# Kernel optimization log

Measured on AMD Instinct MI355X. Metric: run time of the kernel, lower is better.

The kernel has to match this reference:

```python
import math
import jax, jax.numpy as jnp
import numpy as np

EMB = 512
HEADS = 8
NEG_INF = -1e30  # stand-in for -inf that stays finite under softmax


def setup_inputs() -> dict:
    key = jax.random.key(0)
    ks = jax.random.split(key, 6)
    b, t, e, h = 2, 2048, EMB, HEADS
    s = 1.0 / math.sqrt(e)
    return {
        "x": jax.random.normal(ks[0], (b, t, e), dtype=jnp.float32),
        "Wk": jax.random.normal(ks[1], (h * e, e), dtype=jnp.float32) * s,
        "Wq": jax.random.normal(ks[2], (h * e, e), dtype=jnp.float32) * s,
        "Wv": jax.random.normal(ks[3], (h * e, e), dtype=jnp.float32) * s,
        "Wc": jax.random.normal(ks[4], (e, h * e), dtype=jnp.float32) * s,
        "bc": jax.random.normal(ks[5], (e,), dtype=jnp.float32) * 0.01,
    }


def reference(x, Wk, Wq, Wv, Wc, bc):
    b, t, e = x.shape
    h = HEADS
    # projections: Linear(e, h*e) -> (b, t, h, e) -> (b, h, t, e)
    k = (x @ Wk.T).reshape(b, t, h, e).transpose(0, 2, 1, 3)
    q = (x @ Wq.T).reshape(b, t, h, e).transpose(0, 2, 1, 3)
    v = (x @ Wv.T).reshape(b, t, h, e).transpose(0, 2, 1, 3)
    scores = jnp.einsum("bhqe,bhke->bhqk", q, k) / math.sqrt(e)
    # causal mask: strict upper triangle (offset=1) set to -inf
    causal = jnp.tril(jnp.ones((t, t), dtype=bool))  # True where allowed
    scores = jnp.where(causal, scores, NEG_INF)
    weights = jax.nn.softmax(scores, axis=-1)
    out = jnp.einsum("bhqk,bhke->bhqe", weights, v)  # (b, h, t, e)
    out = out.transpose(0, 2, 1, 3).reshape(b, t, h * e)
    return out @ Wc.T + bc
```

## Files before the change

### kernel.cpp

```cpp
#include <hip/hip_runtime.h>

typedef unsigned short u16;
typedef __attribute__((ext_vector_type(4))) short short4v;
typedef __attribute__((ext_vector_type(8))) short short8;
typedef __attribute__((ext_vector_type(4))) float floatx4;

#define GLL16(g, l) __builtin_amdgcn_global_load_lds( \
    (const __attribute__((address_space(1))) void*)(g), \
    (__attribute__((address_space(3))) void*)(l), 16, 0, 0)

__device__ __forceinline__ float b2f(u16 h) {
    union { unsigned u; float f; } v; v.u = ((unsigned)h) << 16; return v.f;
}
__device__ __forceinline__ u16 f2b(float f) {
    union { float f; unsigned u; } v; v.f = f;
    unsigned r = v.u + 0x7fffu + ((v.u >> 16) & 1u);
    return (u16)(r >> 16);
}
__device__ __forceinline__ float launder(float f) {
    return fminf(fmaxf(f, -30000.0f), 30000.0f);
}
__device__ __forceinline__ short8 cvt8(floatx4 a, floatx4 b) {
    short8 v;
    v[0] = (short)f2b(a[0]); v[1] = (short)f2b(a[1]);
    v[2] = (short)f2b(a[2]); v[3] = (short)f2b(a[3]);
    v[4] = (short)f2b(b[0]); v[5] = (short)f2b(b[1]);
    v[6] = (short)f2b(b[2]); v[7] = (short)f2b(b[3]);
    return v;
}

__device__ __forceinline__ int sniff_block(const u16* __restrict__ xs)
{
    __shared__ int cnt;
    if (threadIdx.x == 0) cnt = 0;
    __syncthreads();
    int local = 0;
    for (int i = threadIdx.x; i < 4096; i += 256) {
        const int ex = (xs[i] >> 7) & 0xFF;
        if (ex >= 0x90) ++local;
    }
    if (local) atomicAdd(&cnt, local);
    __syncthreads();
    return cnt > 256;
}

__device__ __forceinline__ void conv_one(const void* __restrict__ raw,
                                         u16* __restrict__ dst, int n, int isf32)
{
    int i = (blockIdx.x * 256 + threadIdx.x) * 8;
    const int stride = gridDim.x * 256 * 8;
    if (isf32) {
        const float* s = (const float*)raw;
        for (; i < n; i += stride)
            *(short8*)(dst + i) = cvt8(*(const floatx4*)(s + i),
                                       *(const floatx4*)(s + i + 4));
    } else {
        const u16* s = (const u16*)raw;
        for (; i < n; i += stride)
            *(short8*)(dst + i) = *(const short8*)(s + i);
    }
}

__global__ __launch_bounds__(256)
void convert4(const void* r0, const void* r1, const void* r2, const void* r3,
              u16* d0, u16* d1, u16* d2, u16* d3, int n, const u16* xs)
{
    const int isf32 = sniff_block(xs);
    const int z = blockIdx.y;
    const void* raw = (z == 0) ? r0 : (z == 1) ? r1 : (z == 2) ? r2 : r3;
    u16* dst        = (z == 0) ? d0 : (z == 1) ? d1 : (z == 2) ? d2 : d3;
    conv_one(raw, dst, n, isf32);
}

__global__ __launch_bounds__(256)
void convert2(const void* r0, const void* r1, u16* d0, u16* d1,
              int n0, int n1, const u16* xs, int* flagp)
{
    const int isf32 = sniff_block(xs);
    if (blockIdx.x == 0 && blockIdx.y == 0 && threadIdx.x == 0) flagp[0] = isf32;
    if (blockIdx.y == 0) conv_one(r0, d0, n0, isf32);
    else                 conv_one(r1, d1, n1, isf32);
}

__global__ __launch_bounds__(256, 2)
void gemm_qkv(const u16* __restrict__ A,
              const u16* __restrict__ B0, const u16* __restrict__ B1, const u16* __restrict__ B2,
              u16* __restrict__ C0, u16* __restrict__ C1, u16* __restrict__ VTout)
{
    const int bid = (blockIdx.x & 7) * 384 + (blockIdx.x >> 3);
    const int z  = bid % 3;
    const int t  = bid / 3;
    const int mx = t & 31;
    const int my = t >> 5;

    const u16* B = (z == 0) ? B0 : ((z == 1) ? B1 : B2);

    __shared__ u16 smem[128 * 136];

    const int tid  = threadIdx.x;
    const int wave = tid >> 6;
    const int lane = tid & 63;
    const int c16  = lane & 15;
    const int quad = lane >> 4;
    const int m0 = mx * 128;
    const int n0 = my * 128;
    const int wm = (wave >> 1) * 64;
    const int wn = (wave & 1) * 64;

    floatx4 acc[4][4] = {};

    const int srow = wave * 32 + (lane >> 2);
    const int scol = (lane & 3) * 8;
    const u16* Ag = A + (size_t)(m0 + srow) * 512 + scol;
    const u16* Bg = B + (size_t)(n0 + srow) * 512 + scol;
    const int woff = (wave * 32) * 32;

    GLL16(Ag,            smem + woff);
    GLL16(Ag + 16 * 512, smem + woff + 16 * 32);
    GLL16(Bg,            smem + 8192 + woff);
    GLL16(Bg + 16 * 512, smem + 8192 + woff + 16 * 32);
    int cur = 0;

    for (int k0 = 0; k0 < 512; k0 += 32) {
        __syncthreads();
        u16* Asc = smem + cur * 4096;
        u16* Bsc = smem + 8192 + cur * 4096;

        if (k0 + 32 < 512) {
            u16* Asn = smem + (cur ^ 1) * 4096;
            u16* Bsn = smem + 8192 + (cur ^ 1) * 4096;
            GLL16(Ag + k0 + 32,            Asn + woff);
            GLL16(Ag + k0 + 32 + 16 * 512, Asn + woff + 16 * 32);
            GLL16(Bg + k0 + 32,            Bsn + woff);
            GLL16(Bg + k0 + 32 + 16 * 512, Bsn + woff + 16 * 32);
        }

        short8 af[4], bf[4];
#pragma unroll
        for (int i = 0; i < 4; ++i)
            af[i] = *(const short8*)&Asc[(wm + i * 16 + c16) * 32 + quad * 8];
#pragma unroll
        for (int i = 0; i < 4; ++i)
            bf[i] = *(const short8*)&Bsc[(wn + i * 16 + c16) * 32 + quad * 8];
#pragma unroll
        for (int i = 0; i < 4; ++i)
#pragma unroll
            for (int j = 0; j < 4; ++j)
                acc[i][j] = __builtin_amdgcn_mfma_f32_16x16x32_bf16(af[i], bf[j], acc[i][j], 0, 0, 0);
        cur ^= 1;
    }

    __syncthreads();

    if (z == 2) {
#pragma unroll
        for (int i = 0; i < 4; ++i)
#pragma unroll
            for (int j = 0; j < 4; ++j) {
                const int lc = wn + j * 16 + c16;
#pragma unroll
                for (int r = 0; r < 4; ++r) {
                    const int lr = wm + i * 16 + quad * 4 + r;
                    smem[lc * 136 + lr] = f2b(launder(acc[i][j][r]));
                }
            }
        __syncthreads();
        const int bq  = m0 >> 11;
        const int tt0 = m0 & 2047;
#pragma unroll
        for (int p = 0; p < 8; ++p) {
            const int lc  = p * 16 + (tid >> 4);
            const int seg = tid & 15;
            const short8 v = *(const short8*)&smem[lc * 136 + seg * 8];
            const int col = n0 + lc;
            const int hh = col >> 9, d = col & 511;
            *(short8*)&VTout[((size_t)((bq * 8 + hh) * 512 + d)) * 2048 + tt0 + seg * 8] = v;
        }
    } else {
        u16* C = (z == 0) ? C0 : C1;
#pragma unroll
        for (int i = 0; i < 4; ++i)
#pragma unroll
            for (int j = 0; j < 4; ++j) {
                const int lc = wn + j * 16 + c16;
#pragma unroll
                for (int r = 0; r < 4; ++r) {
                    const int lr = wm + i * 16 + quad * 4 + r;
                    smem[lr * 136 + lc] = f2b(launder(acc[i][j][r]));
                }
            }
        __syncthreads();
#pragma unroll
        for (int p = 0; p < 8; ++p) {
            const int lr  = p * 16 + (tid >> 4);
            const int seg = tid & 15;
            const short8 v = *(const short8*)&smem[lr * 136 + seg * 8];
            *(short8*)&C[(size_t)(m0 + lr) * 4096 + n0 + seg * 8] = v;
        }
    }
}

__global__ __launch_bounds__(256, 2)
void gemm_out(const u16* __restrict__ A, const u16* __restrict__ B,
              const u16* __restrict__ bias, const int* __restrict__ flagp,
              void* __restrict__ out)
{
    const int bid = (blockIdx.x & 7) * 64 + (blockIdx.x >> 3);
    const int nb = bid & 7;
    const int mb = bid >> 3;

    __shared__ u16 As[2][64 * 32];
    __shared__ u16 Bs[2][64 * 32];

    const int tid  = threadIdx.x;
    const int wave = tid >> 6;
    const int lane = tid & 63;
    const int c16  = lane & 15;
    const int quad = lane >> 4;
    const int m0 = mb * 64;
    const int n0 = nb * 64;
    const int wm = (wave >> 1) * 32;
    const int wn = (wave & 1) * 32;

    floatx4 acc[2][2] = {};

    const int srow = wave * 16 + (lane >> 2);
    const int scol = (lane & 3) * 8;
    const u16* Ag = A + (size_t)(m0 + srow) * 4096 + scol;
    const u16* Bg = B + (size_t)(n0 + srow) * 4096 + scol;
    const int woff = (wave * 16) * 32;

    GLL16(Ag, &As[0][woff]);
    GLL16(Bg, &Bs[0][woff]);
    int cur = 0;

    for (int k0 = 0; k0 < 4096; k0 += 32) {
        __syncthreads();

        if (k0 + 32 < 4096) {
            GLL16(Ag + k0 + 32, &As[cur ^ 1][woff]);
            GLL16(Bg + k0 + 32, &Bs[cur ^ 1][woff]);
        }

        short8 af[2], bf[2];
#pragma unroll
        for (int i = 0; i < 2; ++i)
            af[i] = *(const short8*)&As[cur][(wm + i * 16 + c16) * 32 + quad * 8];
#pragma unroll
        for (int j = 0; j < 2; ++j)
            bf[j] = *(const short8*)&Bs[cur][(wn + j * 16 + c16) * 32 + quad * 8];
#pragma unroll
        for (int i = 0; i < 2; ++i)
#pragma unroll
            for (int j = 0; j < 2; ++j)
                acc[i][j] = __builtin_amdgcn_mfma_f32_16x16x32_bf16(af[i], bf[j], acc[i][j], 0, 0, 0);
        cur ^= 1;
    }

    const int isf32 = flagp[0];
#pragma unroll
    for (int i = 0; i < 2; ++i)
#pragma unroll
        for (int j = 0; j < 2; ++j) {
            const int col = n0 + wn + j * 16 + c16;
            const float bv = b2f(bias[col]);
#pragma unroll
            for (int r = 0; r < 4; ++r) {
                const int row = m0 + wm + i * 16 + quad * 4 + r;
                const float val = launder(acc[i][j][r] + bv);
                if (isf32) ((float*)out)[(size_t)row * 512 + col] = val;
                else       ((u16*)out)[(size_t)row * 512 + col] = f2b(val);
            }
        }
}

#define LOG2E 1.4426950408889634f
#define SM_SCALE 0.044194173824159216f
#define PM 24.0f

__global__ __launch_bounds__(512, 2)
void flash_attn(const u16* __restrict__ Q, const u16* __restrict__ K,
                const u16* __restrict__ VT, u16* __restrict__ O)
{
    __shared__ u16 Ks[2][64 * 516];
    __shared__ u16 Ps[4][16 * 68];
    __shared__ float Lp[2][4][16];

    const int tid  = threadIdx.x;
    const int wave = tid >> 6;
    const int lane = tid & 63;
    const int c16  = lane & 15;
    const int quad = lane >> 4;
    const int g   = wave & 3;
    const int st2 = wave >> 2;

    const int x  = blockIdx.x;
    const int bh = x & 15;
    const int pr = x >> 4;
    const int b  = bh >> 3, h = bh & 7;

    const u16* Qh  = Q  + (size_t)b * 2048 * 4096 + (size_t)h * 512;
    const u16* Kh  = K  + (size_t)b * 2048 * 4096 + (size_t)h * 512;
    const u16* VTh = VT + (size_t)bh * 512 * 2048;
    u16*       Oh  = O  + (size_t)b * 2048 * 4096 + (size_t)h * 512;

#pragma unroll
    for (int i = 0; i < 8; ++i) {
        const int kr = wave * 8 + i;
        GLL16(Kh + (size_t)kr * 4096 + lane * 8, &Ks[0][kr * 516]);
    }
    int cur = 0;

    for (int pm = 0; pm < 2; ++pm) {
        const int qt = pm ? pr : (31 - pr);
        const int q0 = qt * 64;
        const int ntile = qt + 1;
        const int qrow = q0 + g * 16 + c16;
        const int rowq = q0 + g * 16 + quad * 4;

        short8 qf[16];
#pragma unroll
        for (int s = 0; s < 16; ++s)
            qf[s] = *(const short8*)(Qh + (size_t)qrow * 4096 + s * 32 + quad * 8);

        float l_i[4] = {0.0f, 0.0f, 0.0f, 0.0f};
        floatx4 oacc[4][4] = {};

        for (int t = 0; t < ntile; ++t) {
            const int kv0 = t * 64;
            __syncthreads();

            short8 vf[4][2];
            const u16* Vw = VTh + (size_t)(wave * 64) * 2048 + kv0;
#pragma unroll
            for (int dt = 0; dt < 4; ++dt)
#pragma unroll
                for (int ks = 0; ks < 2; ++ks)
                    vf[dt][ks] = *(const short8*)(Vw + (size_t)(dt * 16 + c16) * 2048 + ks * 32 + quad * 8);

            if (t + 1 < ntile || pm == 0) {
                const int knext = (t + 1 < ntile) ? (kv0 + 64) : 0;
#pragma unroll
                for (int i = 0; i < 8; ++i) {
                    const int kr = wave * 8 + i;
                    GLL16(Kh + (size_t)(knext + kr) * 4096 + lane * 8,
                          &Ks[cur ^ 1][kr * 516]);
                }
            }

            floatx4 sv0 = {}, sv1 = {};
            __builtin_amdgcn_s_setprio(1);
#pragma unroll
            for (int s = 0; s < 16; ++s) {
                short8 kf0 = *(const short8*)&Ks[cur][(st2 * 32 + c16) * 516 + s * 32 + quad * 8];
                short8 kf1 = *(const short8*)&Ks[cur][(st2 * 32 + 16 + c16) * 516 + s * 32 + quad * 8];
                sv0 = __builtin_amdgcn_mfma_f32_16x16x32_bf16(qf[s], kf0, sv0, 0, 0, 0);
                sv1 = __builtin_amdgcn_mfma_f32_16x16x32_bf16(qf[s], kf1, sv1, 0, 0, 0);
            }
            __builtin_amdgcn_s_setprio(0);

            const int col0 = kv0 + st2 * 32 + c16;
            if (t + 1 < ntile) {
#pragma unroll
                for (int r = 0; r < 4; ++r) {
                    const float p0 = exp2f((sv0[r] * SM_SCALE - PM) * LOG2E);
                    const float p1 = exp2f((sv1[r] * SM_SCALE - PM) * LOG2E);
                    l_i[r] += p0 + p1;
                    Ps[g][(quad * 4 + r) * 68 + st2 * 32 + c16]      = f2b(p0);
                    Ps[g][(quad * 4 + r) * 68 + st2 * 32 + 16 + c16] = f2b(p1);
                }
            } else {
#pragma unroll
                for (int r = 0; r < 4; ++r) {
                    const float p0 = (col0 > rowq + r)
                        ? 0.0f : exp2f((sv0[r] * SM_SCALE - PM) * LOG2E);
                    const float p1 = (col0 + 16 > rowq + r)
                        ? 0.0f : exp2f((sv1[r] * SM_SCALE - PM) * LOG2E);
                    l_i[r] += p0 + p1;
                    Ps[g][(quad * 4 + r) * 68 + st2 * 32 + c16]      = f2b(p0);
                    Ps[g][(quad * 4 + r) * 68 + st2 * 32 + 16 + c16] = f2b(p1);
                }
            }

            asm volatile("s_waitcnt lgkmcnt(0)" ::: "memory");
            __builtin_amdgcn_s_barrier();
            __builtin_amdgcn_sched_barrier(0);

            __builtin_amdgcn_s_setprio(1);
#pragma unroll
            for (int qg = 0; qg < 4; ++qg) {
                short8 pf0 = *(const short8*)&Ps[qg][c16 * 68 + quad * 8];
                short8 pf1 = *(const short8*)&Ps[qg][c16 * 68 + 32 + quad * 8];
#pragma unroll
                for (int dt = 0; dt < 4; ++dt) {
                    oacc[qg][dt] = __builtin_amdgcn_mfma_f32_16x16x32_bf16(pf0, vf[dt][0], oacc[qg][dt], 0, 0, 0);
                    oacc[qg][dt] = __builtin_amdgcn_mfma_f32_16x16x32_bf16(pf1, vf[dt][1], oacc[qg][dt], 0, 0, 0);
                }
            }
            __builtin_amdgcn_s_setprio(0);

            cur ^= 1;
        }

#pragma unroll
        for (int off = 1; off < 16; off <<= 1)
#pragma unroll
            for (int r = 0; r < 4; ++r)
                l_i[r] += __shfl_xor(l_i[r], off, 16);
        if (c16 == 0) {
#pragma unroll
            for (int r = 0; r < 4; ++r) Lp[st2][g][quad * 4 + r] = l_i[r];
        }
        __syncthreads();

#pragma unroll
        for (int qg = 0; qg < 4; ++qg) {
            float linv[4];
#pragma unroll
            for (int r = 0; r < 4; ++r)
                linv[r] = 1.0f / (Lp[0][qg][quad * 4 + r] + Lp[1][qg][quad * 4 + r]);
#pragma unroll
            for (int dt = 0; dt < 4; ++dt)
#pragma unroll
                for (int r = 0; r < 4; ++r)
                    Oh[(size_t)(q0 + qg * 16 + quad * 4 + r) * 4096 + wave * 64 + dt * 16 + c16] =
                        f2b(launder(oacc[qg][dt][r] * linv[r]));
        }
    }
}

extern "C" void kernel_launch(void* const* d_in, const int* in_sizes, int n_in,
                              void* d_out, int out_size, void* d_ws, size_t ws_size,
                              hipStream_t stream)
{
    const size_t SZ  = (size_t)4096 * 4096;
    const size_t SZh = (size_t)4096 * 512;

    u16* Qb  = (u16*)d_ws;
    u16* Kb  = Qb + SZ;
    u16* Vb  = Kb + SZ;
    u16* VTb = Vb + SZ;
    u16* Ob  = Vb;

    u16* xb  = Vb;
    u16* Wqb = Vb + SZh;
    u16* Wkb = Vb + 2 * SZh;
    u16* Wvb = Vb + 3 * SZh;

    u16* Wcb = Qb;
    u16* bcb = Qb + SZh;
    int* flagp = (int*)(Qb + 2 * SZh);

    const u16* xs = (const u16*)d_in[0];

    convert4<<<dim3(256, 4), 256, 0, stream>>>(
        d_in[0], d_in[2], d_in[1], d_in[3], xb, Wqb, Wkb, Wvb, (int)SZh, xs);

    gemm_qkv<<<dim3(3072), 256, 0, stream>>>(
        xb, Wqb, Wkb, Wvb, Qb, Kb, VTb);

    flash_attn<<<dim3(256), 512, 0, stream>>>(Qb, Kb, VTb, Ob);

    convert2<<<dim3(256, 2), 256, 0, stream>>>(
        d_in[4], d_in[5], Wcb, bcb, (int)SZh, 512, xs, flagp);

    gemm_out<<<dim3(512), 256, 0, stream>>>(Ob, Wcb, bcb, flagp, d_out);
}
```

Before: 370.9 us.

## Split output projection GEMM along K with a separate reduction kernel

The output projection GEMM (4096x512 output, K=4096) is split into four K-slices, each computed by blocks that now use 128x64 tiles. The blocks write fp32 partial sums into the K buffer, which is no longer needed at that point, and a new reduce kernel adds the four slices, applies the bias and converts the output. This is meant to fix the low block count and long serial K loop of the old 512-block kernel, at the cost of extra fp32 partial traffic and one more launch. The occupancy hint on both GEMM kernels is also raised from 2 to 4 blocks.

```diff
diff --git a/kernel.cpp b/kernel.cpp
--- a/kernel.cpp
+++ b/kernel.cpp
@@ -82,7 +82,7 @@
     else                 conv_one(r1, d1, n1, isf32);
 }
 
-__global__ __launch_bounds__(256, 2)
+__global__ __launch_bounds__(256, 4)
 void gemm_qkv(const u16* __restrict__ A,
               const u16* __restrict__ B0, const u16* __restrict__ B1, const u16* __restrict__ B2,
               u16* __restrict__ C0, u16* __restrict__ C1, u16* __restrict__ VTout)
@@ -200,16 +200,16 @@
     }
 }
 
-__global__ __launch_bounds__(256, 2)
-void gemm_out(const u16* __restrict__ A, const u16* __restrict__ B,
-              const u16* __restrict__ bias, const int* __restrict__ flagp,
-              void* __restrict__ out)
-{
-    const int bid = (blockIdx.x & 7) * 64 + (blockIdx.x >> 3);
+__global__ __launch_bounds__(256, 4)
+void gemm_out_partial(const u16* __restrict__ A, const u16* __restrict__ B,
+                      float* __restrict__ Pw)
+{
+    const int bid = blockIdx.x;
     const int nb = bid & 7;
-    const int mb = bid >> 3;
-
-    __shared__ u16 As[2][64 * 32];
+    const int ks = (bid >> 3) & 3;
+    const int mb = bid >> 5;
+
+    __shared__ u16 As[2][128 * 32];
     __shared__ u16 Bs[2][64 * 32];
 
     const int tid  = threadIdx.x;
@@ -217,61 +217,92 @@
     const int lane = tid & 63;
     const int c16  = lane & 15;
     const int quad = lane >> 4;
-    const int m0 = mb * 64;
+    const int m0 = mb * 128;
     const int n0 = nb * 64;
-    const int wm = (wave >> 1) * 32;
+    const int wm = (wave >> 1) * 64;
     const int wn = (wave & 1) * 32;
-
-    floatx4 acc[2][2] = {};
-
-    const int srow = wave * 16 + (lane >> 2);
-    const int scol = (lane & 3) * 8;
-    const u16* Ag = A + (size_t)(m0 + srow) * 4096 + scol;
-    const u16* Bg = B + (size_t)(n0 + srow) * 4096 + scol;
-    const int woff = (wave * 16) * 32;
-
-    GLL16(Ag, &As[0][woff]);
-    GLL16(Bg, &Bs[0][woff]);
+    const int kbase = ks * 1024;
+
+    floatx4 acc[4][2] = {};
+
+    const int srowA = wave * 32 + (lane >> 2);
+    const int srowB = wave * 16 + (lane >> 2);
+    const int scol  = (lane & 3) * 8;
+    const u16* Ag = A + (size_t)(m0 + srowA) * 4096 + kbase + scol;
+    const u16* Bg = B + (size_t)(n0 + srowB) * 4096 + kbase + scol;
+    const int woffA = (wave * 32) * 32;
+    const int woffB = (wave * 16) * 32;
+
+    GLL16(Ag,                     &As[0][woffA]);
+    GLL16(Ag + (size_t)16 * 4096, &As[0][woffA + 16 * 32]);
+    GLL16(Bg,                     &Bs[0][woffB]);
     int cur = 0;
 
-    for (int k0 = 0; k0 < 4096; k0 += 32) {
+    for (int k0 = 0; k0 < 1024; k0 += 32) {
         __syncthreads();
 
-        if (k0 + 32 < 4096) {
-            GLL16(Ag + k0 + 32, &As[cur ^ 1][woff]);
-            GLL16(Bg + k0 + 32, &Bs[cur ^ 1][woff]);
-        }
-
-        short8 af[2], bf[2];
-#pragma unroll
-        for (int i = 0; i < 2; ++i)
+        if (k0 + 32 < 1024) {
+            GLL16(Ag + k0 + 32,                     &As[cur ^ 1][woffA]);
+            GLL16(Ag + k0 + 32 + (size_t)16 * 4096, &As[cur ^ 1][woffA + 16 * 32]);
+            GLL16(Bg + k0 + 32,                     &Bs[cur ^ 1][woffB]);
+        }
+
+        short8 af[4], bf[2];
+#pragma unroll
+        for (int i = 0; i < 4; ++i)
             af[i] = *(const short8*)&As[cur][(wm + i * 16 + c16) * 32 + quad * 8];
 #pragma unroll
         for (int j = 0; j < 2; ++j)
             bf[j] = *(const short8*)&Bs[cur][(wn + j * 16 + c16) * 32 + quad * 8];
 #pragma unroll
-        for (int i = 0; i < 2; ++i)
+        for (int i = 0; i < 4; ++i)
 #pragma unroll
             for (int j = 0; j < 2; ++j)
                 acc[i][j] = __builtin_amdgcn_mfma_f32_16x16x32_bf16(af[i], bf[j], acc[i][j], 0, 0, 0);
         cur ^= 1;
     }
 
-    const int isf32 = flagp[0];
-#pragma unroll
-    for (int i = 0; i < 2; ++i)
+    float* P = Pw + (size_t)ks * 4096 * 512;
+#pragma unroll
+    for (int i = 0; i < 4; ++i)
 #pragma unroll
         for (int j = 0; j < 2; ++j) {
             const int col = n0 + wn + j * 16 + c16;
-            const float bv = b2f(bias[col]);
 #pragma unroll
             for (int r = 0; r < 4; ++r) {
                 const int row = m0 + wm + i * 16 + quad * 4 + r;
-                const float val = launder(acc[i][j][r] + bv);
-                if (isf32) ((float*)out)[(size_t)row * 512 + col] = val;
-                else       ((u16*)out)[(size_t)row * 512 + col] = f2b(val);
-            }
-        }
+                P[(size_t)row * 512 + col] = acc[i][j][r];
+            }
+        }
+}
+
+__global__ __launch_bounds__(256)
+void reduce_out(const float* __restrict__ Pw, const u16* __restrict__ bias,
+                const int* __restrict__ flagp, void* __restrict__ out)
+{
+    const int isf32 = flagp[0];
+    const size_t SL = (size_t)4096 * 512;
+    int g = blockIdx.x * 256 + threadIdx.x;
+    const int stride = gridDim.x * 256;
+    const int ngroups = 4096 * 512 / 4;
+    for (; g < ngroups; g += stride) {
+        const size_t e = (size_t)g * 4;
+        floatx4 s = *(const floatx4*)(Pw + e);
+        s += *(const floatx4*)(Pw + SL + e);
+        s += *(const floatx4*)(Pw + 2 * SL + e);
+        s += *(const floatx4*)(Pw + 3 * SL + e);
+        const int col0 = (g & 127) * 4;
+#pragma unroll
+        for (int r = 0; r < 4; ++r) s[r] = launder(s[r] + b2f(bias[col0 + r]));
+        if (isf32) {
+            *(floatx4*)((float*)out + e) = s;
+        } else {
+            short4v v4;
+#pragma unroll
+            for (int r = 0; r < 4; ++r) v4[r] = (short)f2b(s[r]);
+            *(short4v*)((u16*)out + e) = v4;
+        }
+    }
 }
 
 #define LOG2E 1.4426950408889634f
@@ -450,6 +481,7 @@
     u16* Wcb = Qb;
     u16* bcb = Qb + SZh;
     int* flagp = (int*)(Qb + 2 * SZh);
+    float* Pw  = (float*)Kb;
 
     const u16* xs = (const u16*)d_in[0];
 
@@ -464,5 +496,7 @@
     convert2<<<dim3(256, 2), 256, 0, stream>>>(
         d_in[4], d_in[5], Wcb, bcb, (int)SZh, 512, xs, flagp);
 
-    gemm_out<<<dim3(512), 256, 0, stream>>>(Ob, Wcb, bcb, flagp, d_out);
-}
+    gemm_out_partial<<<dim3(1024), 256, 0, stream>>>(Ob, Wcb, Pw);
+
+    reduce_out<<<dim3(256), 256, 0, stream>>>(Pw, bcb, flagp, d_out);
+}
```

Measured after the change: 357.6 us. -3.6%, faster.
